# Kernel tuning notes

Measured on AMD Instinct MI355X. Metric: run time of the kernel, lower is better.

Reference implementation:

```python
import jax, jax.numpy as jnp
import numpy as np

N_NODES = 50000


def setup_inputs() -> dict:
    key = jax.random.key(0)
    ks = jax.random.split(key, 6)
    nfeat, nhid, hops, nedges = 256, 64, 4, 800000
    x = jax.random.normal(ks[0], (N_NODES, nfeat), dtype=jnp.float32)
    W = jax.random.normal(ks[1], (hops, nfeat, nhid), dtype=jnp.float32) / np.sqrt(nfeat)
    b = jax.random.normal(ks[2], (hops, nhid), dtype=jnp.float32) * 0.01
    adj_rows = jax.random.randint(ks[3], (hops, nedges), 0, N_NODES, dtype=jnp.int32)
    adj_cols = jax.random.randint(ks[4], (hops, nedges), 0, N_NODES, dtype=jnp.int32)
    # normalize-ish positive edge weights, as in a GCN-normalized adjacency
    adj_vals = jax.random.uniform(ks[5], (hops, nedges), dtype=jnp.float32) / 16.0
    return {"x": x, "W": W, "b": b, "adj_rows": adj_rows,
            "adj_cols": adj_cols, "adj_vals": adj_vals}


def reference(x, W, b, adj_rows, adj_cols, adj_vals):
    # SIGN forward (eval mode: dropout = identity).
    # For each hop i: h = x @ W[i] + b[i]; out_i = spmm(adj_i, h)
    # spmm in COO form: out[r] = sum_{e: rows[e]==r} vals[e] * h[cols[e]]
    n = x.shape[0]
    hops = W.shape[0]
    outs = []
    for i in range(hops):  # small fixed hop count (layers+1)
        h = x @ W[i] + b[i]                      # [N, nhid] dense GEMM
        msgs = adj_vals[i][:, None] * h[adj_cols[i]]  # [E, nhid] gather
        outs.append(jax.ops.segment_sum(msgs, adj_rows[i], num_segments=n))
    return jax.nn.elu(jnp.concatenate(outs, axis=1))  # [N, hops*nhid]
```

## Files before the change

### kernel.cpp

```cpp
#include <hip/hip_runtime.h>
#include <hip/hip_bf16.h>
#include <math.h>

#define N_NODES 50000
#define NFEAT 256
#define NHID 64
#define HOPS 4
#define NEDGES 800000
#define NBINS (HOPS * N_NODES)

#define BROWS 256
#define NBUCK 196
#define NBK_ALL (HOPS * NBUCK)
#define CHUNK 8192
#define NCHUNK ((NEDGES + CHUNK - 1) / CHUNK)
#define FS_CAP 8192

#define GM 64
#define LDP 40
#define NGBLK ((N_NODES + GM - 1) / GM)

typedef short bf16x8 __attribute__((ext_vector_type(8)));
typedef float f32x4 __attribute__((ext_vector_type(4)));

static __device__ __forceinline__ unsigned short f2bf(float f) {
    __hip_bfloat16 h = __float2bfloat16(f);
    return *reinterpret_cast<unsigned short*>(&h);
}

__global__ __launch_bounds__(256) void gemm_mfma_kernel(const float* __restrict__ x,
                                                        const float* __restrict__ W,
                                                        const float* __restrict__ b,
                                                        __hip_bfloat16* __restrict__ H) {
    __shared__ unsigned short A_lds[GM * LDP];
    __shared__ unsigned short B_lds[256 * LDP];

    const int t = threadIdx.x;
    const int lane = t & 63;
    const int w = t >> 6;
    const int quad = lane >> 4;
    const int m16 = lane & 15;
    const int row0 = blockIdx.x * GM;

    f32x4 acc[4][4];
#pragma unroll
    for (int mt = 0; mt < 4; ++mt)
#pragma unroll
        for (int nt = 0; nt < 4; ++nt) acc[mt][nt] = (f32x4){0.f, 0.f, 0.f, 0.f};

    for (int ks = 0; ks < 8; ++ks) {
        const int k0 = ks * 32;
#pragma unroll
        for (int it = 0; it < 2; ++it) {
            const int i = t + it * 256;
            const int r = i >> 3;
            const int kq = (i & 7) * 4;
            float4 v = make_float4(0.f, 0.f, 0.f, 0.f);
            if (row0 + r < N_NODES)
                v = *(const float4*)&x[(size_t)(row0 + r) * NFEAT + k0 + kq];
            unsigned short* d = &A_lds[r * LDP + kq];
            d[0] = f2bf(v.x); d[1] = f2bf(v.y); d[2] = f2bf(v.z); d[3] = f2bf(v.w);
        }
#pragma unroll
        for (int it = 0; it < 8; ++it) {
            const int i = t + it * 256;
            const int n4 = i & 63;
            const int kk = i >> 6;
            const int hop = n4 >> 4;
            const int j = (n4 & 15) * 4;
            const float4 v = *(const float4*)&W[(size_t)hop * (NFEAT * NHID)
                                                + (size_t)(k0 + kk) * NHID + j];
            B_lds[(n4 * 4 + 0) * LDP + kk] = f2bf(v.x);
            B_lds[(n4 * 4 + 1) * LDP + kk] = f2bf(v.y);
            B_lds[(n4 * 4 + 2) * LDP + kk] = f2bf(v.z);
            B_lds[(n4 * 4 + 3) * LDP + kk] = f2bf(v.w);
        }
        __syncthreads();

        bf16x8 af[4], bf[4];
#pragma unroll
        for (int mt = 0; mt < 4; ++mt)
            af[mt] = *(const bf16x8*)&A_lds[(mt * 16 + m16) * LDP + quad * 8];
#pragma unroll
        for (int nt = 0; nt < 4; ++nt)
            bf[nt] = *(const bf16x8*)&B_lds[(w * 64 + nt * 16 + m16) * LDP + quad * 8];
#pragma unroll
        for (int mt = 0; mt < 4; ++mt)
#pragma unroll
            for (int nt = 0; nt < 4; ++nt)
                acc[mt][nt] = __builtin_amdgcn_mfma_f32_16x16x32_bf16(
                    af[mt], bf[nt], acc[mt][nt], 0, 0, 0);
        __syncthreads();
    }

#pragma unroll
    for (int nt = 0; nt < 4; ++nt) {
        const int col = w * 64 + nt * 16 + m16;
        const float bias = b[col];
#pragma unroll
        for (int mt = 0; mt < 4; ++mt) {
#pragma unroll
            for (int r = 0; r < 4; ++r) {
                const int row = row0 + mt * 16 + quad * 4 + r;
                if (row < N_NODES)
                    H[(size_t)row * 256 + col] = __float2bfloat16(acc[mt][nt][r] + bias);
            }
        }
    }
}

__global__ __launch_bounds__(256) void bhist_kernel(const int* __restrict__ rows,
                                                    int* __restrict__ bucket_cnt) {
    __shared__ int h[NBUCK];
    const int t = threadIdx.x;
    for (int i = t; i < NBUCK; i += 256) h[i] = 0;
    __syncthreads();
    const int hop = blockIdx.y;
    const int e0 = blockIdx.x * CHUNK;
    const int n = min(CHUNK, NEDGES - e0);
    const size_t base = (size_t)hop * NEDGES + e0;
    for (int i = t; i < n; i += 256) {
        atomicAdd(&h[rows[base + i] >> 8], 1);
    }
    __syncthreads();
    for (int i = t; i < NBUCK; i += 256) {
        if (h[i]) atomicAdd(&bucket_cnt[hop * NBUCK + i], h[i]);
    }
}

__global__ __launch_bounds__(256) void bscan_kernel(const int* __restrict__ cnt,
                                                    int* __restrict__ start,
                                                    int* __restrict__ cursor,
                                                    int* __restrict__ offsets) {
    __shared__ int s[256];
    const int t = threadIdx.x;
    int v[4];
    int tsum = 0;
#pragma unroll
    for (int i = 0; i < 4; ++i) {
        const int idx = t * 4 + i;
        v[i] = (idx < NBK_ALL) ? cnt[idx] : 0;
        tsum += v[i];
    }
    s[t] = tsum;
    __syncthreads();
    for (int off = 1; off < 256; off <<= 1) {
        const int a = (t >= off) ? s[t - off] : 0;
        __syncthreads();
        s[t] += a;
        __syncthreads();
    }
    int run = s[t] - tsum;
#pragma unroll
    for (int i = 0; i < 4; ++i) {
        const int idx = t * 4 + i;
        if (idx < NBK_ALL) {
            start[idx] = run;
            cursor[idx] = run;
            run += v[i];
        }
    }
    if (t == 255) {
        start[NBK_ALL] = run;
        offsets[NBINS] = run;
    }
}

__global__ __launch_bounds__(256) void partition_kernel(const int* __restrict__ rows,
                                                        const int* __restrict__ cols,
                                                        const float* __restrict__ vals,
                                                        int* __restrict__ cursor,
                                                        int2* __restrict__ partbuf) {
    __shared__ int2 pay[CHUNK];
    __shared__ int h[NBUCK], excl[NBUCK], gbase[NBUCK], lcur[NBUCK];
    __shared__ int s[256];
    const int t = threadIdx.x;
    const int hop = blockIdx.y;
    const int e0 = blockIdx.x * CHUNK;
    const int n = min(CHUNK, NEDGES - e0);
    const size_t base = (size_t)hop * NEDGES + e0;

    for (int i = t; i < NBUCK; i += 256) h[i] = 0;
    __syncthreads();

    int myrow[CHUNK / 256];
#pragma unroll
    for (int j = 0; j < CHUNK / 256; ++j) {
        const int i = t + j * 256;
        if (i < n) {
            const int r = rows[base + i];
            myrow[j] = r;
            atomicAdd(&h[r >> 8], 1);
        }
    }
    __syncthreads();

    const int hv = (t < NBUCK) ? h[t] : 0;
    s[t] = hv;
    __syncthreads();
    for (int off = 1; off < 256; off <<= 1) {
        const int a = (t >= off) ? s[t - off] : 0;
        __syncthreads();
        s[t] += a;
        __syncthreads();
    }
    if (t < NBUCK) {
        const int ex = s[t] - hv;
        excl[t] = ex;
        lcur[t] = ex;
        gbase[t] = hv ? atomicAdd(&cursor[hop * NBUCK + t], hv) : 0;
    }
    __syncthreads();

#pragma unroll
    for (int j = 0; j < CHUNK / 256; ++j) {
        const int i = t + j * 256;
        if (i < n) {
            const int r = myrow[j];
            const int c = cols[base + i];
            const float v = vals[base + i];
            const int pos = atomicAdd(&lcur[r >> 8], 1);
            pay[pos] = make_int2((r << 16) | c, __float_as_int(v));
        }
    }
    __syncthreads();

    for (int i = t; i < n; i += 256) {
        const int2 p = pay[i];
        const int bk = ((unsigned)p.x) >> 24;
        partbuf[gbase[bk] + (i - excl[bk])] = p;
    }
}

__global__ __launch_bounds__(256) void fsort_kernel(const int* __restrict__ start,
                                                    int2* __restrict__ partbuf,
                                                    int* __restrict__ offsets) {
    __shared__ int2 pay[FS_CAP];
    __shared__ int h[BROWS], excl[BROWS], cur[BROWS];
    __shared__ int s[256];
    const int t = threadIdx.x;
    const int hop = blockIdx.y;
    const int bucket = blockIdx.x;
    const int g = hop * NBUCK + bucket;
    const int s0 = start[g];
    const int n = min(start[g + 1] - s0, FS_CAP);

    h[t] = 0;
    __syncthreads();

    for (int i = t; i < n; i += 256) {
        const int2 p = partbuf[s0 + i];
        pay[i] = p;
        atomicAdd(&h[((unsigned)p.x >> 16) & 255], 1);
    }
    __syncthreads();

    const int hv = h[t];
    s[t] = hv;
    __syncthreads();
    for (int off = 1; off < 256; off <<= 1) {
        const int a = (t >= off) ? s[t - off] : 0;
        __syncthreads();
        s[t] += a;
        __syncthreads();
    }
    const int ex = s[t] - hv;
    excl[t] = ex;
    cur[t] = 0;
    const int row = bucket * BROWS + t;
    if (row < N_NODES) offsets[hop * N_NODES + row] = s0 + ex;
    __syncthreads();

    for (int i = t; i < n; i += 256) {
        const int2 p = pay[i];
        const int rl = ((unsigned)p.x >> 16) & 255;
        const int pos = s0 + excl[rl] + atomicAdd(&cur[rl], 1);
        partbuf[pos] = make_int2(p.x & 0xFFFF, p.y);
    }
}

__global__ __launch_bounds__(256) void gather_kernel(const __hip_bfloat16* __restrict__ H,
                                                     const int* __restrict__ offsets,
                                                     const int2* __restrict__ epk,
                                                     float* __restrict__ out) {
    const int row = blockIdx.x;
    const int hop = threadIdx.x >> 6;
    const int lane = threadIdx.x & 63;
    const int e8 = lane >> 3;
    const int f8 = lane & 7;
    const int bin = hop * N_NODES + row;
    const int s = offsets[bin];
    const int e2 = offsets[bin + 1];
    const char* Hb = (const char*)H;
    const int hbase = (hop << 7) + (f8 << 4);

    float acc[8];
#pragma unroll
    for (int j = 0; j < 8; ++j) acc[j] = 0.f;

    for (int g = s; g < e2; g += 64) {
        int2 p = make_int2(0, 0);
        const int eidx = g + lane;
        if (eidx < e2) p = epk[eidx];
        const int nit = min(8, (e2 - g + 7) >> 3);
        for (int it = 0; it < nit; ++it) {
            const int src = it * 8 + e8;
            const int col = __shfl(p.x, src, 64);
            const float val = __int_as_float(__shfl(p.y, src, 64));
            const uint4 hv = *(const uint4*)(Hb + ((size_t)col << 9) + hbase);
            const unsigned u[4] = {hv.x, hv.y, hv.z, hv.w};
#pragma unroll
            for (int q = 0; q < 4; ++q) {
                const float lo = __uint_as_float(u[q] << 16);
                const float hi = __uint_as_float(u[q] & 0xffff0000u);
                acc[q * 2]     = fmaf(val, lo, acc[q * 2]);
                acc[q * 2 + 1] = fmaf(val, hi, acc[q * 2 + 1]);
            }
        }
    }

#pragma unroll
    for (int m = 8; m <= 32; m <<= 1) {
#pragma unroll
        for (int j = 0; j < 8; ++j) acc[j] += __shfl_xor(acc[j], m, 64);
    }

    if (lane < 8) {
#pragma unroll
        for (int j = 0; j < 8; ++j)
            acc[j] = acc[j] > 0.f ? acc[j] : expf(acc[j]) - 1.f;
        float4* dst = (float4*)&out[(size_t)row * 256 + hop * 64 + lane * 8];
        dst[0] = make_float4(acc[0], acc[1], acc[2], acc[3]);
        dst[1] = make_float4(acc[4], acc[5], acc[6], acc[7]);
    }
}

#define EPW 8
__global__ __launch_bounds__(256) void scatter_kernel(const __hip_bfloat16* __restrict__ H,
                                                      const int* __restrict__ rows,
                                                      const int* __restrict__ cols,
                                                      const float* __restrict__ vals,
                                                      float* __restrict__ out) {
    const int lane = threadIdx.x & 63;
    const int wid = __builtin_amdgcn_readfirstlane(threadIdx.x >> 6);
    const int hop = blockIdx.y;
    const int e0 = (blockIdx.x * 4 + wid) * EPW;
    const int base = hop * NEDGES;
    const int hoff = hop * 64 + lane;
#pragma unroll
    for (int i = 0; i < EPW; ++i) {
        const int e = e0 + i;
        const int r = rows[base + e];
        const int c = cols[base + e];
        const float v = vals[base + e];
        unsafeAtomicAdd(&out[(size_t)r * 256 + hoff],
                        v * __bfloat162float(H[(size_t)c * 256 + hoff]));
    }
}

__global__ __launch_bounds__(256) void elu_kernel(float* __restrict__ out, int n4) {
    const int i = blockIdx.x * 256 + threadIdx.x;
    if (i < n4) {
        float4 v = ((float4*)out)[i];
        v.x = v.x > 0.f ? v.x : expf(v.x) - 1.f;
        v.y = v.y > 0.f ? v.y : expf(v.y) - 1.f;
        v.z = v.z > 0.f ? v.z : expf(v.z) - 1.f;
        v.w = v.w > 0.f ? v.w : expf(v.w) - 1.f;
        ((float4*)out)[i] = v;
    }
}

extern "C" void kernel_launch(void* const* d_in, const int* in_sizes, int n_in,
                              void* d_out, int out_size, void* d_ws, size_t ws_size,
                              hipStream_t stream) {
    const float* x        = (const float*)d_in[0];
    const float* W        = (const float*)d_in[1];
    const float* b        = (const float*)d_in[2];
    const int*   adj_rows = (const int*)d_in[3];
    const int*   adj_cols = (const int*)d_in[4];
    const float* adj_vals = (const float*)d_in[5];
    float* out = (float*)d_out;

    char* w = (char*)d_ws;
    size_t off = 0;
    __hip_bfloat16* H = (__hip_bfloat16*)(w + off);
    off += (size_t)N_NODES * 256 * 2;
    int2*  partbuf    = (int2*)(w + off);  off += (size_t)HOPS * NEDGES * 8;
    int*   offsets    = (int*)(w + off);   off += (((size_t)(NBINS + 1)) * 4 + 255) & ~255ull;
    int*   bucket_cnt = (int*)(w + off);   off += ((size_t)NBK_ALL * 4 + 255) & ~255ull;
    int*   bstart     = (int*)(w + off);   off += (((size_t)NBK_ALL + 1) * 4 + 255) & ~255ull;
    int*   bcursor    = (int*)(w + off);   off += ((size_t)NBK_ALL * 4 + 255) & ~255ull;
    const bool use_sorted = (ws_size >= off);

    gemm_mfma_kernel<<<NGBLK, 256, 0, stream>>>(x, W, b, H);

    if (use_sorted) {
        hipMemsetAsync(bucket_cnt, 0, (size_t)NBK_ALL * 4, stream);
        bhist_kernel<<<dim3(NCHUNK, HOPS), 256, 0, stream>>>(adj_rows, bucket_cnt);
        bscan_kernel<<<1, 256, 0, stream>>>(bucket_cnt, bstart, bcursor, offsets);
        partition_kernel<<<dim3(NCHUNK, HOPS), 256, 0, stream>>>(adj_rows, adj_cols,
                                                                 adj_vals, bcursor, partbuf);
        fsort_kernel<<<dim3(NBUCK, HOPS), 256, 0, stream>>>(bstart, partbuf, offsets);
        gather_kernel<<<N_NODES, 256, 0, stream>>>(H, offsets, partbuf, out);
    } else {
        hipMemsetAsync(d_out, 0, (size_t)out_size * sizeof(float), stream);
        scatter_kernel<<<dim3(NEDGES / (4 * EPW), HOPS), 256, 0, stream>>>(
            H, adj_rows, adj_cols, adj_vals, out);
        elu_kernel<<<(out_size / 4 + 255) / 256, 256, 0, stream>>>(out, out_size / 4);
    }
}
```

Baseline: 366.7 us.

## Replace per-row sort and gather with bucketed LDS-accumulating gather

Bucket width drops from 256 to 64 rows. The fine per-row sort kernel and the per-row gather are removed and replaced by one kernel per bucket that accumulates edge contributions into a 64x64 shared-memory tile with LDS atomics, then applies ELU and writes the output. This drops one full pass over the partition buffer and the offsets array, at the cost of shared-memory atomic contention and scalar 2-byte H loads per lane instead of 16-byte vector loads. The bucket prefix scans are widened to cover more buckets.

```diff
diff --git a/kernel.cpp b/kernel.cpp
--- a/kernel.cpp
+++ b/kernel.cpp
@@ -7,14 +7,12 @@
 #define NHID 64
 #define HOPS 4
 #define NEDGES 800000
-#define NBINS (HOPS * N_NODES)
-
-#define BROWS 256
-#define NBUCK 196
+
+#define BROWS 64
+#define NBUCK 782
 #define NBK_ALL (HOPS * NBUCK)
 #define CHUNK 8192
 #define NCHUNK ((NEDGES + CHUNK - 1) / CHUNK)
-#define FS_CAP 8192
 
 #define GM 64
 #define LDP 40
@@ -120,7 +118,7 @@
     const int n = min(CHUNK, NEDGES - e0);
     const size_t base = (size_t)hop * NEDGES + e0;
     for (int i = t; i < n; i += 256) {
-        atomicAdd(&h[rows[base + i] >> 8], 1);
+        atomicAdd(&h[rows[base + i] >> 6], 1);
     }
     __syncthreads();
     for (int i = t; i < NBUCK; i += 256) {
@@ -128,17 +126,17 @@
     }
 }
 
+#define SCAN_V ((NBK_ALL + 255) / 256)
 __global__ __launch_bounds__(256) void bscan_kernel(const int* __restrict__ cnt,
                                                     int* __restrict__ start,
-                                                    int* __restrict__ cursor,
-                                                    int* __restrict__ offsets) {
+                                                    int* __restrict__ cursor) {
     __shared__ int s[256];
     const int t = threadIdx.x;
-    int v[4];
+    int v[SCAN_V];
     int tsum = 0;
 #pragma unroll
-    for (int i = 0; i < 4; ++i) {
-        const int idx = t * 4 + i;
+    for (int i = 0; i < SCAN_V; ++i) {
+        const int idx = t * SCAN_V + i;
         v[i] = (idx < NBK_ALL) ? cnt[idx] : 0;
         tsum += v[i];
     }
@@ -152,18 +150,15 @@
     }
     int run = s[t] - tsum;
 #pragma unroll
-    for (int i = 0; i < 4; ++i) {
-        const int idx = t * 4 + i;
+    for (int i = 0; i < SCAN_V; ++i) {
+        const int idx = t * SCAN_V + i;
         if (idx < NBK_ALL) {
             start[idx] = run;
             cursor[idx] = run;
             run += v[i];
         }
     }
-    if (t == 255) {
-        start[NBK_ALL] = run;
-        offsets[NBINS] = run;
-    }
+    if (t == 255) start[NBK_ALL] = run;
 }
 
 __global__ __launch_bounds__(256) void partition_kernel(const int* __restrict__ rows,
@@ -190,13 +185,20 @@
         if (i < n) {
             const int r = rows[base + i];
             myrow[j] = r;
-            atomicAdd(&h[r >> 8], 1);
-        }
-    }
-    __syncthreads();
-
-    const int hv = (t < NBUCK) ? h[t] : 0;
-    s[t] = hv;
+            atomicAdd(&h[r >> 6], 1);
+        }
+    }
+    __syncthreads();
+
+    int pv[4];
+    int tsum = 0;
+#pragma unroll
+    for (int i = 0; i < 4; ++i) {
+        const int idx = t * 4 + i;
+        pv[i] = (idx < NBUCK) ? h[idx] : 0;
+        tsum += pv[i];
+    }
+    s[t] = tsum;
     __syncthreads();
     for (int off = 1; off < 256; off <<= 1) {
         const int a = (t >= off) ? s[t - off] : 0;
@@ -204,11 +206,16 @@
         s[t] += a;
         __syncthreads();
     }
-    if (t < NBUCK) {
-        const int ex = s[t] - hv;
-        excl[t] = ex;
-        lcur[t] = ex;
-        gbase[t] = hv ? atomicAdd(&cursor[hop * NBUCK + t], hv) : 0;
+    int run = s[t] - tsum;
+#pragma unroll
+    for (int i = 0; i < 4; ++i) {
+        const int idx = t * 4 + i;
+        if (idx < NBUCK) {
+            excl[idx] = run;
+            lcur[idx] = run;
+            gbase[idx] = pv[i] ? atomicAdd(&cursor[hop * NBUCK + idx], pv[i]) : 0;
+            run += pv[i];
+        }
     }
     __syncthreads();
 
@@ -219,7 +226,7 @@
             const int r = myrow[j];
             const int c = cols[base + i];
             const float v = vals[base + i];
-            const int pos = atomicAdd(&lcur[r >> 8], 1);
+            const int pos = atomicAdd(&lcur[r >> 6], 1);
             pay[pos] = make_int2((r << 16) | c, __float_as_int(v));
         }
     }
@@ -227,111 +234,66 @@
 
     for (int i = t; i < n; i += 256) {
         const int2 p = pay[i];
-        const int bk = ((unsigned)p.x) >> 24;
+        const int bk = ((unsigned)p.x) >> 22;
         partbuf[gbase[bk] + (i - excl[bk])] = p;
     }
 }
 
-__global__ __launch_bounds__(256) void fsort_kernel(const int* __restrict__ start,
-                                                    int2* __restrict__ partbuf,
-                                                    int* __restrict__ offsets) {
-    __shared__ int2 pay[FS_CAP];
-    __shared__ int h[BROWS], excl[BROWS], cur[BROWS];
-    __shared__ int s[256];
-    const int t = threadIdx.x;
+__global__ __launch_bounds__(256) void bgather_kernel(const __hip_bfloat16* __restrict__ H,
+                                                      const int* __restrict__ start,
+                                                      const int2* __restrict__ partbuf,
+                                                      float* __restrict__ out) {
+    __shared__ float acc[BROWS * NHID];
+    const int t = threadIdx.x;
+    const int f = t & 63;
+    const int wid = __builtin_amdgcn_readfirstlane(t >> 6);
     const int hop = blockIdx.y;
     const int bucket = blockIdx.x;
     const int g = hop * NBUCK + bucket;
     const int s0 = start[g];
-    const int n = min(start[g + 1] - s0, FS_CAP);
-
-    h[t] = 0;
-    __syncthreads();
-
-    for (int i = t; i < n; i += 256) {
-        const int2 p = partbuf[s0 + i];
-        pay[i] = p;
-        atomicAdd(&h[((unsigned)p.x >> 16) & 255], 1);
-    }
-    __syncthreads();
-
-    const int hv = h[t];
-    s[t] = hv;
-    __syncthreads();
-    for (int off = 1; off < 256; off <<= 1) {
-        const int a = (t >= off) ? s[t - off] : 0;
-        __syncthreads();
-        s[t] += a;
-        __syncthreads();
-    }
-    const int ex = s[t] - hv;
-    excl[t] = ex;
-    cur[t] = 0;
-    const int row = bucket * BROWS + t;
-    if (row < N_NODES) offsets[hop * N_NODES + row] = s0 + ex;
-    __syncthreads();
-
-    for (int i = t; i < n; i += 256) {
-        const int2 p = pay[i];
-        const int rl = ((unsigned)p.x >> 16) & 255;
-        const int pos = s0 + excl[rl] + atomicAdd(&cur[rl], 1);
-        partbuf[pos] = make_int2(p.x & 0xFFFF, p.y);
-    }
-}
-
-__global__ __launch_bounds__(256) void gather_kernel(const __hip_bfloat16* __restrict__ H,
-                                                     const int* __restrict__ offsets,
-                                                     const int2* __restrict__ epk,
-                                                     float* __restrict__ out) {
-    const int row = blockIdx.x;
-    const int hop = threadIdx.x >> 6;
-    const int lane = threadIdx.x & 63;
-    const int e8 = lane >> 3;
-    const int f8 = lane & 7;
-    const int bin = hop * N_NODES + row;
-    const int s = offsets[bin];
-    const int e2 = offsets[bin + 1];
-    const char* Hb = (const char*)H;
-    const int hbase = (hop << 7) + (f8 << 4);
-
-    float acc[8];
-#pragma unroll
-    for (int j = 0; j < 8; ++j) acc[j] = 0.f;
-
-    for (int g = s; g < e2; g += 64) {
-        int2 p = make_int2(0, 0);
-        const int eidx = g + lane;
-        if (eidx < e2) p = epk[eidx];
-        const int nit = min(8, (e2 - g + 7) >> 3);
-        for (int it = 0; it < nit; ++it) {
-            const int src = it * 8 + e8;
-            const int col = __shfl(p.x, src, 64);
-            const float val = __int_as_float(__shfl(p.y, src, 64));
-            const uint4 hv = *(const uint4*)(Hb + ((size_t)col << 9) + hbase);
-            const unsigned u[4] = {hv.x, hv.y, hv.z, hv.w};
-#pragma unroll
-            for (int q = 0; q < 4; ++q) {
-                const float lo = __uint_as_float(u[q] << 16);
-                const float hi = __uint_as_float(u[q] & 0xffff0000u);
-                acc[q * 2]     = fmaf(val, lo, acc[q * 2]);
-                acc[q * 2 + 1] = fmaf(val, hi, acc[q * 2 + 1]);
-            }
-        }
-    }
-
-#pragma unroll
-    for (int m = 8; m <= 32; m <<= 1) {
-#pragma unroll
-        for (int j = 0; j < 8; ++j) acc[j] += __shfl_xor(acc[j], m, 64);
-    }
-
-    if (lane < 8) {
-#pragma unroll
-        for (int j = 0; j < 8; ++j)
-            acc[j] = acc[j] > 0.f ? acc[j] : expf(acc[j]) - 1.f;
-        float4* dst = (float4*)&out[(size_t)row * 256 + hop * 64 + lane * 8];
-        dst[0] = make_float4(acc[0], acc[1], acc[2], acc[3]);
-        dst[1] = make_float4(acc[4], acc[5], acc[6], acc[7]);
+    const int s1 = start[g + 1];
+
+    for (int i = t * 4; i < BROWS * NHID; i += 1024)
+        *(float4*)&acc[i] = make_float4(0.f, 0.f, 0.f, 0.f);
+    __syncthreads();
+
+    const unsigned short* Hf = (const unsigned short*)H + hop * 64 + f;
+
+    int e0 = s0 + wid * 8;
+    for (; e0 + 8 <= s1; e0 += 32) {
+        int2 p[8];
+#pragma unroll
+        for (int i = 0; i < 8; ++i) p[i] = partbuf[e0 + i];
+#pragma unroll
+        for (int i = 0; i < 8; ++i) {
+            const int rlow = (((unsigned)p[i].x) >> 16) & (BROWS - 1);
+            const int col = p[i].x & 0xffff;
+            const float val = __int_as_float(p[i].y);
+            const float hv = __uint_as_float(((unsigned)Hf[(size_t)col << 8]) << 16);
+            atomicAdd(&acc[rlow * NHID + f], val * hv);
+        }
+    }
+    for (int e = e0; e < s1 && e < e0 + 8; ++e) {
+        const int2 p = partbuf[e];
+        const int rlow = (((unsigned)p.x) >> 16) & (BROWS - 1);
+        const int col = p.x & 0xffff;
+        const float val = __int_as_float(p.y);
+        const float hv = __uint_as_float(((unsigned)Hf[(size_t)col << 8]) << 16);
+        atomicAdd(&acc[rlow * NHID + f], val * hv);
+    }
+
+    __syncthreads();
+
+    const int row0 = bucket * BROWS;
+#pragma unroll
+    for (int k = 0; k < BROWS / 4; ++k) {
+        const int r = wid * (BROWS / 4) + k;
+        const int grow = row0 + r;
+        if (grow < N_NODES) {
+            float v = acc[r * NHID + f];
+            v = v > 0.f ? v : expf(v) - 1.f;
+            out[(size_t)grow * 256 + hop * 64 + f] = v;
+        }
     }
 }
 
@@ -386,7 +348,6 @@
     __hip_bfloat16* H = (__hip_bfloat16*)(w + off);
     off += (size_t)N_NODES * 256 * 2;
     int2*  partbuf    = (int2*)(w + off);  off += (size_t)HOPS * NEDGES * 8;
-    int*   offsets    = (int*)(w + off);   off += (((size_t)(NBINS + 1)) * 4 + 255) & ~255ull;
     int*   bucket_cnt = (int*)(w + off);   off += ((size_t)NBK_ALL * 4 + 255) & ~255ull;
     int*   bstart     = (int*)(w + off);   off += (((size_t)NBK_ALL + 1) * 4 + 255) & ~255ull;
     int*   bcursor    = (int*)(w + off);   off += ((size_t)NBK_ALL * 4 + 255) & ~255ull;
@@ -397,11 +358,10 @@
     if (use_sorted) {
         hipMemsetAsync(bucket_cnt, 0, (size_t)NBK_ALL * 4, stream);
         bhist_kernel<<<dim3(NCHUNK, HOPS), 256, 0, stream>>>(adj_rows, bucket_cnt);
-        bscan_kernel<<<1, 256, 0, stream>>>(bucket_cnt, bstart, bcursor, offsets);
+        bscan_kernel<<<1, 256, 0, stream>>>(bucket_cnt, bstart, bcursor);
         partition_kernel<<<dim3(NCHUNK, HOPS), 256, 0, stream>>>(adj_rows, adj_cols,
                                                                  adj_vals, bcursor, partbuf);
-        fsort_kernel<<<dim3(NBUCK, HOPS), 256, 0, stream>>>(bstart, partbuf, offsets);
-        gather_kernel<<<N_NODES, 256, 0, stream>>>(H, offsets, partbuf, out);
+        bgather_kernel<<<dim3(NBUCK, HOPS), 256, 0, stream>>>(H, bstart, partbuf, out);
     } else {
         hipMemsetAsync(d_out, 0, (size_t)out_size * sizeof(float), stream);
         scatter_kernel<<<dim3(NEDGES / (4 * EPW), HOPS), 256, 0, stream>>>(
```

Result: slower. 1.355 ms (+269.6%).

## Pre-cast inputs to bf16 for GEMM and rewrite CSR gather per row

Applied to the files above, without the earlier changes.

Adds kernels that cast x and a transposed W to bf16 in workspace buffers, and a GEMM that reads these bf16 operands instead of converting fp32 on the fly. The per-node gather kernel is replaced by one where each wave handles 16 rows of one hop, with one lane per feature, broadcasting edge indices via readlane and loading 2-byte H elements. This aims to cut GEMM load bandwidth and conversion work and to raise gather parallelism. In exchange it adds an extra pass over x and uses narrow scalar loads per lane in the gather. The cast buffers reuse partbuf and offsets, which are only overwritten after the GEMM consumes them.

```diff
diff --git a/kernel.cpp b/kernel.cpp
--- a/kernel.cpp
+++ b/kernel.cpp
@@ -26,6 +26,100 @@
 static __device__ __forceinline__ unsigned short f2bf(float f) {
     __hip_bfloat16 h = __float2bfloat16(f);
     return *reinterpret_cast<unsigned short*>(&h);
+}
+
+__global__ __launch_bounds__(256) void castx_kernel(const float* __restrict__ x,
+                                                    unsigned short* __restrict__ Xbf) {
+    const int i = blockIdx.x * 256 + threadIdx.x;
+    const size_t base = (size_t)i * 8;
+    if (base < (size_t)N_NODES * NFEAT) {
+        const float4 a = *(const float4*)&x[base];
+        const float4 c = *(const float4*)&x[base + 4];
+        unsigned short o[8] = {f2bf(a.x), f2bf(a.y), f2bf(a.z), f2bf(a.w),
+                               f2bf(c.x), f2bf(c.y), f2bf(c.z), f2bf(c.w)};
+        *(bf16x8*)&Xbf[base] = *(const bf16x8*)o;
+    }
+}
+
+__global__ __launch_bounds__(256) void castw_kernel(const float* __restrict__ W,
+                                                    unsigned short* __restrict__ Wt) {
+    const int idx = blockIdx.x * 256 + threadIdx.x;
+    if (idx < HOPS * NFEAT * NHID) {
+        const int hop = idx >> 14;
+        const int k = (idx >> 6) & 255;
+        const int c = idx & 63;
+        Wt[((size_t)(hop * 64 + c)) * NFEAT + k] = f2bf(W[idx]);
+    }
+}
+
+__global__ __launch_bounds__(256) void gemm_bf_kernel(const unsigned short* __restrict__ Xbf,
+                                                      const unsigned short* __restrict__ Wt,
+                                                      const float* __restrict__ b,
+                                                      __hip_bfloat16* __restrict__ H) {
+    __shared__ unsigned short A_lds[GM * LDP];
+    __shared__ unsigned short B_lds[256 * LDP];
+
+    const int t = threadIdx.x;
+    const int lane = t & 63;
+    const int w = t >> 6;
+    const int quad = lane >> 4;
+    const int m16 = lane & 15;
+    const int row0 = blockIdx.x * GM;
+
+    f32x4 acc[4][4];
+#pragma unroll
+    for (int mt = 0; mt < 4; ++mt)
+#pragma unroll
+        for (int nt = 0; nt < 4; ++nt) acc[mt][nt] = (f32x4){0.f, 0.f, 0.f, 0.f};
+
+    for (int ks = 0; ks < 8; ++ks) {
+        const int k0 = ks * 32;
+        {
+            const int r = t >> 2;
+            const int kq = (t & 3) * 8;
+            bf16x8 v = {0, 0, 0, 0, 0, 0, 0, 0};
+            if (row0 + r < N_NODES)
+                v = *(const bf16x8*)&Xbf[(size_t)(row0 + r) * NFEAT + k0 + kq];
+            *(bf16x8*)&A_lds[r * LDP + kq] = v;
+        }
+#pragma unroll
+        for (int q = 0; q < 4; ++q) {
+            const int kq = q * 8;
+            const bf16x8 v = *(const bf16x8*)&Wt[(size_t)t * NFEAT + k0 + kq];
+            *(bf16x8*)&B_lds[t * LDP + kq] = v;
+        }
+        __syncthreads();
+
+        bf16x8 af[4], bf[4];
+#pragma unroll
+        for (int mt = 0; mt < 4; ++mt)
+            af[mt] = *(const bf16x8*)&A_lds[(mt * 16 + m16) * LDP + quad * 8];
+#pragma unroll
+        for (int nt = 0; nt < 4; ++nt)
+            bf[nt] = *(const bf16x8*)&B_lds[(w * 64 + nt * 16 + m16) * LDP + quad * 8];
+#pragma unroll
+        for (int mt = 0; mt < 4; ++mt)
+#pragma unroll
+            for (int nt = 0; nt < 4; ++nt)
+                acc[mt][nt] = __builtin_amdgcn_mfma_f32_16x16x32_bf16(
+                    af[mt], bf[nt], acc[mt][nt], 0, 0, 0);
+        __syncthreads();
+    }
+
+#pragma unroll
+    for (int nt = 0; nt < 4; ++nt) {
+        const int col = w * 64 + nt * 16 + m16;
+        const float bias = b[col];
+#pragma unroll
+        for (int mt = 0; mt < 4; ++mt) {
+#pragma unroll
+            for (int r = 0; r < 4; ++r) {
+                const int row = row0 + mt * 16 + quad * 4 + r;
+                if (row < N_NODES)
+                    H[(size_t)row * 256 + col] = __float2bfloat16(acc[mt][nt][r] + bias);
+            }
+        }
+    }
 }
 
 __global__ __launch_bounds__(256) void gemm_mfma_kernel(const float* __restrict__ x,
@@ -279,59 +373,54 @@
     }
 }
 
-__global__ __launch_bounds__(256) void gather_kernel(const __hip_bfloat16* __restrict__ H,
-                                                     const int* __restrict__ offsets,
-                                                     const int2* __restrict__ epk,
-                                                     float* __restrict__ out) {
-    const int row = blockIdx.x;
-    const int hop = threadIdx.x >> 6;
-    const int lane = threadIdx.x & 63;
-    const int e8 = lane >> 3;
-    const int f8 = lane & 7;
-    const int bin = hop * N_NODES + row;
-    const int s = offsets[bin];
-    const int e2 = offsets[bin + 1];
-    const char* Hb = (const char*)H;
-    const int hbase = (hop << 7) + (f8 << 4);
-
-    float acc[8];
-#pragma unroll
-    for (int j = 0; j < 8; ++j) acc[j] = 0.f;
-
-    for (int g = s; g < e2; g += 64) {
-        int2 p = make_int2(0, 0);
-        const int eidx = g + lane;
-        if (eidx < e2) p = epk[eidx];
-        const int nit = min(8, (e2 - g + 7) >> 3);
-        for (int it = 0; it < nit; ++it) {
-            const int src = it * 8 + e8;
-            const int col = __shfl(p.x, src, 64);
-            const float val = __int_as_float(__shfl(p.y, src, 64));
-            const uint4 hv = *(const uint4*)(Hb + ((size_t)col << 9) + hbase);
-            const unsigned u[4] = {hv.x, hv.y, hv.z, hv.w};
-#pragma unroll
-            for (int q = 0; q < 4; ++q) {
-                const float lo = __uint_as_float(u[q] << 16);
-                const float hi = __uint_as_float(u[q] & 0xffff0000u);
-                acc[q * 2]     = fmaf(val, lo, acc[q * 2]);
-                acc[q * 2 + 1] = fmaf(val, hi, acc[q * 2 + 1]);
+__global__ __launch_bounds__(256) void csr_gather_kernel(const __hip_bfloat16* __restrict__ H,
+                                                         const int* __restrict__ offsets,
+                                                         const int2* __restrict__ epk,
+                                                         float* __restrict__ out) {
+    const int t = threadIdx.x;
+    const int f = t & 63;
+    const int w = t >> 6;
+    const int hop = blockIdx.y;
+    const int row0w = blockIdx.x * 64 + w * 16;
+    if (row0w >= N_NODES) return;
+    const int bin0 = hop * N_NODES + row0w;
+
+    int off_l = 0;
+    if (f <= 16) off_l = offsets[bin0 + f];
+
+    const unsigned short* Hf = (const unsigned short*)H + hop * 64 + f;
+    float* outp = out + (size_t)row0w * 256 + hop * 64 + f;
+
+    for (int r = 0; r < 16; ++r) {
+        const int s  = __builtin_amdgcn_readlane(off_l, r);
+        const int e2 = __builtin_amdgcn_readlane(off_l, r + 1);
+        float acc = 0.f;
+        int e = s;
+        for (; e + 8 <= e2; e += 8) {
+            const int2 m = epk[e + (f & 7)];
+            float h8[8];
+#pragma unroll
+            for (int j = 0; j < 8; ++j) {
+                const int col = __builtin_amdgcn_readlane(m.x, j);
+                h8[j] = __uint_as_float((unsigned)Hf[(size_t)col << 8] << 16);
             }
-        }
-    }
-
-#pragma unroll
-    for (int m = 8; m <= 32; m <<= 1) {
-#pragma unroll
-        for (int j = 0; j < 8; ++j) acc[j] += __shfl_xor(acc[j], m, 64);
-    }
-
-    if (lane < 8) {
-#pragma unroll
-        for (int j = 0; j < 8; ++j)
-            acc[j] = acc[j] > 0.f ? acc[j] : expf(acc[j]) - 1.f;
-        float4* dst = (float4*)&out[(size_t)row * 256 + hop * 64 + lane * 8];
-        dst[0] = make_float4(acc[0], acc[1], acc[2], acc[3]);
-        dst[1] = make_float4(acc[4], acc[5], acc[6], acc[7]);
+#pragma unroll
+            for (int j = 0; j < 8; ++j) {
+                const float val = __uint_as_float((unsigned)__builtin_amdgcn_readlane(m.y, j));
+                acc = fmaf(val, h8[j], acc);
+            }
+        }
+        if (e < e2) {
+            const int2 m = epk[e + (f & 7)];
+            const int rem = e2 - e;
+            for (int j = 0; j < rem; ++j) {
+                const int col = __builtin_amdgcn_readlane(m.x, j);
+                const float val = __uint_as_float((unsigned)__builtin_amdgcn_readlane(m.y, j));
+                acc = fmaf(val, __uint_as_float((unsigned)Hf[(size_t)col << 8] << 16), acc);
+            }
+        }
+        acc = acc > 0.f ? acc : expf(acc) - 1.f;
+        outp[(size_t)r * 256] = acc;
     }
 }
 
@@ -392,17 +481,24 @@
     int*   bcursor    = (int*)(w + off);   off += ((size_t)NBK_ALL * 4 + 255) & ~255ull;
     const bool use_sorted = (ws_size >= off);
 
-    gemm_mfma_kernel<<<NGBLK, 256, 0, stream>>>(x, W, b, H);
+    unsigned short* Xbf = (unsigned short*)partbuf;
+    unsigned short* Wt  = (unsigned short*)offsets;
 
     if (use_sorted) {
+        castx_kernel<<<(N_NODES * NFEAT / 8 + 255) / 256, 256, 0, stream>>>(x, Xbf);
+        castw_kernel<<<(HOPS * NFEAT * NHID + 255) / 256, 256, 0, stream>>>(W, Wt);
+        gemm_bf_kernel<<<NGBLK, 256, 0, stream>>>(Xbf, Wt, b, H);
+
         hipMemsetAsync(bucket_cnt, 0, (size_t)NBK_ALL * 4, stream);
         bhist_kernel<<<dim3(NCHUNK, HOPS), 256, 0, stream>>>(adj_rows, bucket_cnt);
         bscan_kernel<<<1, 256, 0, stream>>>(bucket_cnt, bstart, bcursor, offsets);
         partition_kernel<<<dim3(NCHUNK, HOPS), 256, 0, stream>>>(adj_rows, adj_cols,
                                                                  adj_vals, bcursor, partbuf);
         fsort_kernel<<<dim3(NBUCK, HOPS), 256, 0, stream>>>(bstart, partbuf, offsets);
-        gather_kernel<<<N_NODES, 256, 0, stream>>>(H, offsets, partbuf, out);
+        csr_gather_kernel<<<dim3((N_NODES + 63) / 64, HOPS), 256, 0, stream>>>(
+            H, offsets, partbuf, out);
     } else {
+        gemm_mfma_kernel<<<NGBLK, 256, 0, stream>>>(x, W, b, H);
         hipMemsetAsync(d_out, 0, (size_t)out_size * sizeof(float), stream);
         scatter_kernel<<<dim3(NEDGES / (4 * EPW), HOPS), 256, 0, stream>>>(
             H, adj_rows, adj_cols, adj_vals, out);
```

New measurement: 361.5 us. About the same (-1.4%).
